# Kernel optimization log

Hardware: AMD Instinct MI355X
Metric: run time of the kernel (lower is better)

The kernel has to match this reference:

```python
import jax, jax.numpy as jnp
import numpy as np

B, S, D = 4, 2048, 1024

def setup_inputs() -> dict:
    key = jax.random.key(0)
    kx, kq, kk, kv = jax.random.split(key, 4)
    glorot = (6.0 / (D + D)) ** 0.5
    return {
        "x": jax.random.normal(kx, (B, S, D), dtype=jnp.float32),
        "Wq": jax.random.uniform(kq, (D, D), jnp.float32, -glorot, glorot),
        "Wk": jax.random.uniform(kk, (D, D), jnp.float32, -glorot, glorot),
        "Wv": jax.random.uniform(kv, (D, D), jnp.float32, -glorot, glorot),
    }

def reference(x, Wq, Wk, Wv):
    # q,k,v: [B,S,D]
    q = jnp.einsum("bsd,de->bse", x, Wq)
    k = jnp.einsum("bsd,de->bse", x, Wk)
    v = jnp.einsum("bsd,de->bse", x, Wv)
    scale = jnp.sqrt(jnp.asarray(q.shape[-1], q.dtype))
    scores = jnp.einsum("bqd,bkd->bqk", q, k) / scale  # [B,S,S]
    w = jax.nn.softmax(scores, axis=-1)
    return jnp.einsum("bqk,bkd->bqd", w, v)
```

## Files before the change

kernel.cpp:

```cpp
#include <hip/hip_runtime.h>
#include <hip/hip_bf16.h>


typedef _Float16 half_t;
typedef _Float16 half8 __attribute__((ext_vector_type(8)));
typedef _Float16 half4v __attribute__((ext_vector_type(4)));
typedef float f32x4 __attribute__((ext_vector_type(4)));

__device__ __forceinline__ void load16_to_lds(const half_t* g, half_t* l) {
  __builtin_amdgcn_global_load_lds(
      (const __attribute__((address_space(1))) void*)g,
      (__attribute__((address_space(3))) void*)l,
      16, 0, 0);
}

template <typename OutT>
__global__ __launch_bounds__(256) void gemm_nt(
    const half_t* __restrict__ A, const half_t* __restrict__ Bm,
    OutT* __restrict__ C, int lda, int ldb, int ldc,
    long long sA, long long sB, long long sC, int K, float scale) {
  __shared__ __align__(16) half_t As[128 * 64];
  __shared__ __align__(16) half_t Bs[128 * 64];

  A  += (long long)blockIdx.z * sA;
  Bm += (long long)blockIdx.z * sB;
  C  += (long long)blockIdx.z * sC;

  const int t    = threadIdx.x;
  const int m0   = blockIdx.y * 128;
  const int n0   = blockIdx.x * 128;
  const int wave = t >> 6;
  const int lane = t & 63;
  const int wm   = (wave >> 1) * 64;
  const int wn   = (wave & 1) * 64;
  const int lm   = lane & 15;
  const int lq   = lane >> 4;
  const int lswz = lm & 7;

  const int trow = t >> 3;
  const int tchk = (t & 7) ^ (trow & 7);

  const half_t* gA0 = A  + (size_t)(m0 + trow) * lda + tchk * 8;
  const half_t* gB0 = Bm + (size_t)(n0 + trow) * ldb + tchk * 8;
  const size_t stepA = (size_t)32 * lda;
  const size_t stepB = (size_t)32 * ldb;

  half_t* lA0 = &As[t * 8];
  half_t* lB0 = &Bs[t * 8];

  f32x4 acc[4][4] = {};

  for (int k0 = 0; k0 < K; k0 += 64) {
    __syncthreads();
#pragma unroll
    for (int n = 0; n < 4; ++n) {
      load16_to_lds(gA0 + n * stepA + k0, lA0 + n * 2048);
      load16_to_lds(gB0 + n * stepB + k0, lB0 + n * 2048);
    }
    __syncthreads();

    for (int kk = 0; kk < 2; ++kk) {
      const int pos = ((kk * 4 + lq) ^ lswz) * 8;
      half8 a[4], b[4];
#pragma unroll
      for (int i = 0; i < 4; ++i)
        a[i] = *(const half8*)&As[(wm + i * 16 + lm) * 64 + pos];
#pragma unroll
      for (int j = 0; j < 4; ++j)
        b[j] = *(const half8*)&Bs[(wn + j * 16 + lm) * 64 + pos];
#pragma unroll
      for (int i = 0; i < 4; ++i)
#pragma unroll
        for (int j = 0; j < 4; ++j)
          acc[i][j] = __builtin_amdgcn_mfma_f32_16x16x32_f16(a[i], b[j], acc[i][j], 0, 0, 0);
    }
  }

#pragma unroll
  for (int i = 0; i < 4; ++i) {
#pragma unroll
    for (int j = 0; j < 4; ++j) {
      const int col = n0 + wn + j * 16 + lm;
#pragma unroll
      for (int r = 0; r < 4; ++r) {
        const int row = m0 + wm + i * 16 + lq * 4 + r;
        C[(size_t)row * ldc + col] = (OutT)(acc[i][j][r] * scale);
      }
    }
  }
}

__global__ __launch_bounds__(256) void cast_f32_to_f16(
    const float* __restrict__ in, half_t* __restrict__ out, int n) {
  int i = (blockIdx.x * 256 + threadIdx.x) * 4;
  if (i >= n) return;
  const float4 v = *reinterpret_cast<const float4*>(in + i);
  half4v o;
  o.x = (half_t)v.x; o.y = (half_t)v.y; o.z = (half_t)v.z; o.w = (half_t)v.w;
  *reinterpret_cast<half4v*>(out + i) = o;
}

__global__ __launch_bounds__(256) void cast_transpose(
    const float* __restrict__ in, half_t* __restrict__ out, int rows, int cols) {
  __shared__ half_t tile[32][33];
  const int r0 = blockIdx.y * 32, c0 = blockIdx.x * 32;
  const int tx = threadIdx.x & 31, ty = threadIdx.x >> 5;
#pragma unroll
  for (int i = 0; i < 32; i += 8)
    tile[ty + i][tx] = (half_t)in[(size_t)(r0 + ty + i) * cols + c0 + tx];
  __syncthreads();
#pragma unroll
  for (int i = 0; i < 32; i += 8)
    out[(size_t)(c0 + ty + i) * rows + r0 + tx] = tile[tx][ty + i];
}

__global__ __launch_bounds__(256) void transpose_f16(
    const half_t* __restrict__ in, half_t* __restrict__ out,
    int ldin, int rows, long long sIn, long long sOut) {
  __shared__ half_t tile[32][33];
  const half_t* ib = in + (long long)blockIdx.z * sIn;
  half_t* ob = out + (long long)blockIdx.z * sOut;
  const int r0 = blockIdx.y * 32, c0 = blockIdx.x * 32;
  const int tx = threadIdx.x & 31, ty = threadIdx.x >> 5;
#pragma unroll
  for (int i = 0; i < 32; i += 8)
    tile[ty + i][tx] = ib[(size_t)(r0 + ty + i) * ldin + c0 + tx];
  __syncthreads();
#pragma unroll
  for (int i = 0; i < 32; i += 8)
    ob[(size_t)(c0 + ty + i) * rows + r0 + tx] = tile[tx][ty + i];
}

__global__ __launch_bounds__(256) void softmax_rows(
    half_t* __restrict__ S, int n, long long sBatch) {
  half_t* row = S + (long long)blockIdx.y * sBatch + (size_t)blockIdx.x * n;
  const int t = threadIdx.x;
  half8 hv = *(const half8*)(row + t * 8);

  float vals[8];
  float m = -1e30f;
#pragma unroll
  for (int i = 0; i < 8; ++i) {
    vals[i] = (float)hv[i];
    m = fmaxf(m, vals[i]);
  }
#pragma unroll
  for (int off = 32; off; off >>= 1) m = fmaxf(m, __shfl_xor(m, off));
  __shared__ float redm[4];
  if ((t & 63) == 0) redm[t >> 6] = m;
  __syncthreads();
  m = fmaxf(fmaxf(redm[0], redm[1]), fmaxf(redm[2], redm[3]));

  float s = 0.f;
#pragma unroll
  for (int i = 0; i < 8; ++i) {
    vals[i] = __expf(vals[i] - m);
    s += vals[i];
  }
#pragma unroll
  for (int off = 32; off; off >>= 1) s += __shfl_xor(s, off);
  __shared__ float reds[4];
  if ((t & 63) == 0) reds[t >> 6] = s;
  __syncthreads();
  s = reds[0] + reds[1] + reds[2] + reds[3];
  const float inv = 1.0f / s;

  half8 o;
#pragma unroll
  for (int i = 0; i < 8; ++i) o[i] = (half_t)(vals[i] * inv);
  *(half8*)(row + t * 8) = o;
}

extern "C" void kernel_launch(void* const* d_in, const int* in_sizes, int n_in,
                              void* d_out, int out_size, void* d_ws, size_t ws_size,
                              hipStream_t stream) {
  constexpr int Bb = 4, S = 2048, D = 1024;
  constexpr int N3 = 3 * D;
  constexpr size_t MS = (size_t)Bb * S;

  const float* x  = (const float*)d_in[0];
  const float* Wq = (const float*)d_in[1];
  const float* Wk = (const float*)d_in[2];
  const float* Wv = (const float*)d_in[3];
  float* out = (float*)d_out;

  char* p = (char*)d_ws;
  half_t* xh  = (half_t*)p; p += MS * D * 2;
  half_t* wt  = (half_t*)p; p += (size_t)N3 * D * 2;
  half_t* qkv = (half_t*)p; p += MS * (size_t)N3 * 2;
  half_t* vt  = (half_t*)p; p += MS * D * 2;
  half_t* sc  = (half_t*)p; p += (size_t)Bb * S * S * 2;

  cast_f32_to_f16<<<(MS * D) / 1024, 256, 0, stream>>>(x, xh, (int)(MS * D));
  dim3 gT(D / 32, D / 32);
  cast_transpose<<<gT, 256, 0, stream>>>(Wq, wt + 0 * (size_t)D * D, D, D);
  cast_transpose<<<gT, 256, 0, stream>>>(Wk, wt + 1 * (size_t)D * D, D, D);
  cast_transpose<<<gT, 256, 0, stream>>>(Wv, wt + 2 * (size_t)D * D, D, D);

  gemm_nt<half_t><<<dim3(N3 / 128, MS / 128), 256, 0, stream>>>(
      xh, wt, qkv, D, D, N3, 0, 0, 0, D, 1.0f);

  transpose_f16<<<dim3(D / 32, S / 32, Bb), 256, 0, stream>>>(
      qkv + 2 * D, vt, N3, S, (long long)S * N3, (long long)D * S);

  gemm_nt<half_t><<<dim3(S / 128, S / 128, Bb), 256, 0, stream>>>(
      qkv + 0 * D, qkv + 1 * D, sc, N3, N3, S,
      (long long)S * N3, (long long)S * N3, (long long)S * S, D, 1.0f / 32.0f);

  softmax_rows<<<dim3(S, Bb), 256, 0, stream>>>(sc, S, (long long)S * S);

  gemm_nt<float><<<dim3(D / 128, S / 128, Bb), 256, 0, stream>>>(
      sc, vt, out, S, S, D,
      (long long)S * S, (long long)D * S, (long long)S * D, S, 1.0f);
}
```

Before: 275.0 us.

## Use 256x128 GEMM tiles with 32x32x16 MFMA instructions

New measurement: 283.8 us. 1.03x slower.

```diff
diff --git a/kernel.cpp b/kernel.cpp
--- a/kernel.cpp
+++ b/kernel.cpp
@@ -5,7 +5,7 @@
 typedef _Float16 half_t;
 typedef _Float16 half8 __attribute__((ext_vector_type(8)));
 typedef _Float16 half4v __attribute__((ext_vector_type(4)));
-typedef float f32x4 __attribute__((ext_vector_type(4)));
+typedef float f32x16 __attribute__((ext_vector_type(16)));
 
 __device__ __forceinline__ void load16_to_lds(const half_t* g, half_t* l) {
   __builtin_amdgcn_global_load_lds(
@@ -15,11 +15,11 @@
 }
 
 template <typename OutT>
-__global__ __launch_bounds__(256) void gemm_nt(
+__global__ __launch_bounds__(256, 2) void gemm_nt(
     const half_t* __restrict__ A, const half_t* __restrict__ Bm,
     OutT* __restrict__ C, int lda, int ldb, int ldc,
     long long sA, long long sB, long long sC, int K, float scale) {
-  __shared__ __align__(16) half_t As[128 * 64];
+  __shared__ __align__(16) half_t As[256 * 64];
   __shared__ __align__(16) half_t Bs[128 * 64];
 
   A  += (long long)blockIdx.z * sA;
@@ -27,15 +27,15 @@
   C  += (long long)blockIdx.z * sC;
 
   const int t    = threadIdx.x;
-  const int m0   = blockIdx.y * 128;
+  const int m0   = blockIdx.y * 256;
   const int n0   = blockIdx.x * 128;
   const int wave = t >> 6;
   const int lane = t & 63;
-  const int wm   = (wave >> 1) * 64;
+  const int wm   = (wave >> 1) * 128;
   const int wn   = (wave & 1) * 64;
-  const int lm   = lane & 15;
-  const int lq   = lane >> 4;
-  const int lswz = lm & 7;
+  const int ln   = lane & 31;
+  const int hl   = lane >> 5;
+  const int lswz = ln & 7;
 
   const int trow = t >> 3;
   const int tchk = (t & 7) ^ (trow & 7);
@@ -48,43 +48,49 @@
   half_t* lA0 = &As[t * 8];
   half_t* lB0 = &Bs[t * 8];
 
-  f32x4 acc[4][4] = {};
+  f32x16 acc[4][2] = {};
 
   for (int k0 = 0; k0 < K; k0 += 64) {
     __syncthreads();
 #pragma unroll
-    for (int n = 0; n < 4; ++n) {
+    for (int n = 0; n < 8; ++n)
       load16_to_lds(gA0 + n * stepA + k0, lA0 + n * 2048);
+#pragma unroll
+    for (int n = 0; n < 4; ++n)
       load16_to_lds(gB0 + n * stepB + k0, lB0 + n * 2048);
+    __syncthreads();
+
+#pragma unroll
+    for (int kk = 0; kk < 4; ++kk) {
+      const int c = kk * 2 + hl;
+      half8 a[4], b[2];
+#pragma unroll
+      for (int i = 0; i < 4; ++i) {
+        const int R = wm + i * 32 + ln;
+        a[i] = *(const half8*)&As[R * 64 + (c ^ lswz) * 8];
+      }
+#pragma unroll
+      for (int j = 0; j < 2; ++j) {
+        const int R = wn + j * 32 + ln;
+        b[j] = *(const half8*)&Bs[R * 64 + (c ^ lswz) * 8];
+      }
+#pragma unroll
+      for (int i = 0; i < 4; ++i)
+#pragma unroll
+        for (int j = 0; j < 2; ++j)
+          acc[i][j] = __builtin_amdgcn_mfma_f32_32x32x16_f16(a[i], b[j], acc[i][j], 0, 0, 0);
     }
-    __syncthreads();
-
-    for (int kk = 0; kk < 2; ++kk) {
-      const int pos = ((kk * 4 + lq) ^ lswz) * 8;
-      half8 a[4], b[4];
-#pragma unroll
-      for (int i = 0; i < 4; ++i)
-        a[i] = *(const half8*)&As[(wm + i * 16 + lm) * 64 + pos];
-#pragma unroll
-      for (int j = 0; j < 4; ++j)
-        b[j] = *(const half8*)&Bs[(wn + j * 16 + lm) * 64 + pos];
-#pragma unroll
-      for (int i = 0; i < 4; ++i)
-#pragma unroll
-        for (int j = 0; j < 4; ++j)
-          acc[i][j] = __builtin_amdgcn_mfma_f32_16x16x32_f16(a[i], b[j], acc[i][j], 0, 0, 0);
-    }
   }
 
 #pragma unroll
   for (int i = 0; i < 4; ++i) {
 #pragma unroll
-    for (int j = 0; j < 4; ++j) {
-      const int col = n0 + wn + j * 16 + lm;
-#pragma unroll
-      for (int r = 0; r < 4; ++r) {
-        const int row = m0 + wm + i * 16 + lq * 4 + r;
-        C[(size_t)row * ldc + col] = (OutT)(acc[i][j][r] * scale);
+    for (int j = 0; j < 2; ++j) {
+      const int col = n0 + wn + j * 32 + ln;
+#pragma unroll
+      for (int reg = 0; reg < 16; ++reg) {
+        const int row = m0 + wm + i * 32 + 4 * hl + (reg & 3) + 8 * (reg >> 2);
+        C[(size_t)row * ldc + col] = (OutT)(acc[i][j][reg] * scale);
       }
     }
   }
@@ -197,19 +203,19 @@
   cast_transpose<<<gT, 256, 0, stream>>>(Wk, wt + 1 * (size_t)D * D, D, D);
   cast_transpose<<<gT, 256, 0, stream>>>(Wv, wt + 2 * (size_t)D * D, D, D);
 
-  gemm_nt<half_t><<<dim3(N3 / 128, MS / 128), 256, 0, stream>>>(
+  gemm_nt<half_t><<<dim3(N3 / 128, MS / 256), 256, 0, stream>>>(
       xh, wt, qkv, D, D, N3, 0, 0, 0, D, 1.0f);
 
   transpose_f16<<<dim3(D / 32, S / 32, Bb), 256, 0, stream>>>(
       qkv + 2 * D, vt, N3, S, (long long)S * N3, (long long)D * S);
 
-  gemm_nt<half_t><<<dim3(S / 128, S / 128, Bb), 256, 0, stream>>>(
+  gemm_nt<half_t><<<dim3(S / 128, S / 256, Bb), 256, 0, stream>>>(
       qkv + 0 * D, qkv + 1 * D, sc, N3, N3, S,
       (long long)S * N3, (long long)S * N3, (long long)S * S, D, 1.0f / 32.0f);
 
   softmax_rows<<<dim3(S, Bb), 256, 0, stream>>>(sc, S, (long long)S * S);
 
-  gemm_nt<float><<<dim3(D / 128, S / 128, Bb), 256, 0, stream>>>(
+  gemm_nt<float><<<dim3(D / 128, S / 256, Bb), 256, 0, stream>>>(
       sc, vt, out, S, S, D,
       (long long)S * S, (long long)D * S, (long long)S * D, S, 1.0f);
 }
```
